# Kernel optimization log

Measured on AMD Instinct MI355X. Metric: run time of the kernel, lower is better.

Reference implementation:

```python
import jax, jax.numpy as jnp
import numpy as np

D = 4096


def ste_sign(v):
    # forward: sign(v); backward: identity (straight-through)
    return v + jax.lax.stop_gradient(jnp.sign(v) - v)


def setup_inputs() -> dict:
    key = jax.random.key(0)
    ks = jax.random.split(key, 7)
    B, T = 2, 4096
    x = jax.random.normal(ks[0], (B, T, D), dtype=jnp.float32)
    role_write = jax.random.normal(ks[1], (D,), dtype=jnp.float32) * 0.02
    role_read = jax.random.normal(ks[2], (D,), dtype=jnp.float32) * 0.02
    # nn.Linear(D, 1): weight (1, D) stored here as (D,), bias scalar (1,)
    lim = 1.0 / np.sqrt(D)
    wg_w = jax.random.uniform(ks[3], (D,), dtype=jnp.float32, minval=-lim, maxval=lim)
    wg_b = jax.random.uniform(ks[4], (1,), dtype=jnp.float32, minval=-lim, maxval=lim)
    rg_w = jax.random.uniform(ks[5], (D,), dtype=jnp.float32, minval=-lim, maxval=lim)
    rg_b = jax.random.uniform(ks[6], (1,), dtype=jnp.float32, minval=-lim, maxval=lim)
    return {"x": x, "role_write": role_write, "role_read": role_read,
            "wg_w": wg_w, "wg_b": wg_b, "rg_w": rg_w, "rg_b": rg_b}


def reference(x, role_write, role_read, wg_w, wg_b, rg_w, rg_b):
    # ---- write: gated sign-bind facts, causal bundle via cumsum over T ----
    signs = ste_sign(x)                                  # (B,T,D)
    facts = signs * ste_sign(role_write)                 # bind with write role
    w_gate = jax.nn.sigmoid(jnp.einsum('btd,d->bt', x, wg_w) + wg_b[0])
    gated_facts = facts * w_gate[..., None]
    memory = jnp.cumsum(gated_facts, axis=1)             # (B,T,D) causal bundle
    # ---- read: unbind memory with query, gated residual add ----
    query = signs * ste_sign(role_read)
    retrieved = ste_sign(memory) * query
    r_gate = jax.nn.sigmoid(jnp.einsum('btd,d->bt', x, rg_w) + rg_b[0])
    return x + r_gate[..., None] * retrieved
```

## Files before the change

### kernel.cpp

```cpp
#include <hip/hip_runtime.h>
#include <math.h>


#define T_LEN 4096
#define D_LEN 4096
#define TC 32
#define NC (T_LEN / TC)
#define D4 (D_LEN / 4)

typedef float nfloat4 __attribute__((ext_vector_type(4)));

__device__ __forceinline__ float fsgn(float v) {
    return (v > 0.f) ? 1.f : ((v < 0.f) ? -1.f : 0.f);
}
__device__ __forceinline__ double dsgn(double v) {
    return (v > 0.) ? 1. : ((v < 0.) ? -1. : 0.);
}
__device__ __forceinline__ unsigned scode(float v) {
    return (v > 0.f) ? 2u : ((v < 0.f) ? 0u : 1u);
}

__global__ __launch_bounds__(1024) void gates_partial_kernel(
    const float* __restrict__ x,
    const float* __restrict__ wg_w, const float* __restrict__ wg_b,
    const float* __restrict__ rg_w, const float* __restrict__ rg_b,
    double* __restrict__ wgate, double* __restrict__ rgate,
    double* __restrict__ partial)
{
    const int c = blockIdx.x;
    const int b = blockIdx.y;
    const int tid = threadIdx.x;

    __shared__ unsigned char codes[TC][D4];
    __shared__ double wg_s[TC];
    __shared__ double rg_s[TC];

    const int r  = tid >> 5;
    const int k0 = tid & 31;
    const float4* xr = (const float4*)(x + ((size_t)b * T_LEN + (size_t)c * TC + r) * D_LEN);
    const float4* w4 = (const float4*)wg_w;
    const float4* g4 = (const float4*)rg_w;

    double dw = 0., dg = 0.;
    #pragma unroll 4
    for (int j = 0; j < 32; ++j) {
        const int idx = k0 + j * 32;
        float4 v = xr[idx];
        float4 a = w4[idx];
        float4 g = g4[idx];
        dw += (double)v.x * a.x + (double)v.y * a.y
            + (double)v.z * a.z + (double)v.w * a.w;
        dg += (double)v.x * g.x + (double)v.y * g.y
            + (double)v.z * g.z + (double)v.w * g.w;
        codes[r][idx] = (unsigned char)(scode(v.x) | (scode(v.y) << 2)
                                      | (scode(v.z) << 4) | (scode(v.w) << 6));
    }
    #pragma unroll
    for (int off = 16; off >= 1; off >>= 1) {
        dw += __shfl_down(dw, off, 32);
        dg += __shfl_down(dg, off, 32);
    }
    if (k0 == 0) {
        wg_s[r] = 1. / (1. + exp(-(dw + (double)wg_b[0])));
        rg_s[r] = 1. / (1. + exp(-(dg + (double)rg_b[0])));
    }
    __syncthreads();

    if (tid < TC) {
        const int row = b * T_LEN + c * TC + tid;
        wgate[row] = wg_s[tid];
        rgate[row] = rg_s[tid];
    }

    double a0 = 0., a1 = 0., a2 = 0., a3 = 0.;
    #pragma unroll 8
    for (int t = 0; t < TC; ++t) {
        unsigned code = codes[t][tid];
        double w = wg_s[t];
        a0 += (double)((int)( code       & 3u) - 1) * w;
        a1 += (double)((int)((code >> 2) & 3u) - 1) * w;
        a2 += (double)((int)((code >> 4) & 3u) - 1) * w;
        a3 += (double)((int)((code >> 6) & 3u) - 1) * w;
    }
    double* rec = partial + ((size_t)(b * NC + c)) * D_LEN + tid * 4;
    rec[0] = a0; rec[1] = a1; rec[2] = a2; rec[3] = a3;
}

__global__ __launch_bounds__(256) void prefix_kernel(
    const double* __restrict__ partial, double* __restrict__ prefix)
{
    const int m = blockIdx.x * 256 + threadIdx.x;
    const int b = blockIdx.y;
    double s = 0.;
    for (int c = 0; c < NC; ++c) {
        size_t idx = ((size_t)(b * NC + c)) * D_LEN + m;
        double v = partial[idx];
        prefix[idx] = s;
        s += v;
    }
}

__global__ __launch_bounds__(256) void final_kernel(
    const float* __restrict__ x,
    const double* __restrict__ wgate, const double* __restrict__ rgate,
    const float* __restrict__ role_w, const float* __restrict__ role_r,
    const double* __restrict__ prefix,
    float* __restrict__ out)
{
    const int b = blockIdx.z;
    const int c = blockIdx.y;
    const int d4 = blockIdx.x * 256 + threadIdx.x;

    __shared__ double wsm[TC];
    __shared__ float rsm[TC];
    if (threadIdx.x < TC) {
        wsm[threadIdx.x] = wgate[b * T_LEN + c * TC + threadIdx.x];
        rsm[threadIdx.x] = (float)rgate[b * T_LEN + c * TC + threadIdx.x];
    }
    __syncthreads();

    float4 rw = ((const float4*)role_w)[d4];
    float4 rr = ((const float4*)role_r)[d4];
    const float kx = fsgn(rw.x) * fsgn(rr.x);
    const float ky = fsgn(rw.y) * fsgn(rr.y);
    const float kz = fsgn(rw.z) * fsgn(rr.z);
    const float kw = fsgn(rw.w) * fsgn(rr.w);

    const double* p = prefix + ((size_t)(b * NC + c)) * D_LEN + d4 * 4;
    double ax = p[0], ay = p[1], az = p[2], aw = p[3];

    const float4* x4 = (const float4*)x;
    nfloat4* o4 = (nfloat4*)out;
    const size_t slab = ((size_t)b * T_LEN + (size_t)c * TC) * D4 + d4;

    #pragma unroll 4
    for (int i = 0; i < TC; ++i) {
        float4 v = x4[slab + (size_t)i * D4];
        double w = wsm[i];
        float rf = rsm[i];
        float sx = fsgn(v.x), sy = fsgn(v.y), sz = fsgn(v.z), sw2 = fsgn(v.w);
        ax += (double)sx * w; ay += (double)sy * w;
        az += (double)sz * w; aw += (double)sw2 * w;
        nfloat4 o;
        o.x = v.x + rf * kx * (float)dsgn(ax) * sx;
        o.y = v.y + rf * ky * (float)dsgn(ay) * sy;
        o.z = v.z + rf * kz * (float)dsgn(az) * sz;
        o.w = v.w + rf * kw * (float)dsgn(aw) * sw2;
        __builtin_nontemporal_store(o, &o4[slab + (size_t)i * D4]);
    }
}

extern "C" void kernel_launch(void* const* d_in, const int* in_sizes, int n_in,
                              void* d_out, int out_size, void* d_ws, size_t ws_size,
                              hipStream_t stream) {
    const float* x      = (const float*)d_in[0];
    const float* role_w = (const float*)d_in[1];
    const float* role_r = (const float*)d_in[2];
    const float* wg_w   = (const float*)d_in[3];
    const float* wg_b   = (const float*)d_in[4];
    const float* rg_w   = (const float*)d_in[5];
    const float* rg_b   = (const float*)d_in[6];
    float* out = (float*)d_out;

    const int B = in_sizes[0] / (T_LEN * D_LEN);
    const int BT = B * T_LEN;

    double* wgate   = (double*)d_ws;
    double* rgate   = wgate + BT;
    double* partial = rgate + BT;
    double* prefix  = partial + (size_t)B * NC * D_LEN;

    dim3 g12(NC, B);
    gates_partial_kernel<<<g12, 1024, 0, stream>>>(
        x, wg_w, wg_b, rg_w, rg_b, wgate, rgate, partial);

    dim3 g2b(D_LEN / 256, B);
    prefix_kernel<<<g2b, 256, 0, stream>>>(partial, prefix);

    dim3 g3(D4 / 256, NC, B);
    final_kernel<<<g3, 256, 0, stream>>>(
        x, wgate, rgate, role_w, role_r, prefix, out);
}
```

Before: 88.82 us.

## Halve time-chunk size and parallelize chunk prefix scan across sections

Chunk length drops from 32 to 16 rows, so the gates/partial kernel launches twice as many blocks, each handling 16 rows with a full 64-lane wavefront per row. The prefix kernel, which walked all chunks serially with one thread per column, now splits the chunks into 8 sections per column. Each section is summed independently, combined with a shuffle scan, and then written. The aim is to expose more parallelism in the serial prefix pass, at the cost of twice the partial/prefix workspace traffic and two reads of partial in the scan.

```diff
diff --git a/kernel.cpp b/kernel.cpp
--- a/kernel.cpp
+++ b/kernel.cpp
@@ -4,9 +4,11 @@
 
 #define T_LEN 4096
 #define D_LEN 4096
-#define TC 32
+#define TC 16
 #define NC (T_LEN / TC)
 #define D4 (D_LEN / 4)
+#define NSEC 8
+#define SEC (NC / NSEC)
 
 typedef float nfloat4 __attribute__((ext_vector_type(4)));
 
@@ -35,16 +37,16 @@
     __shared__ double wg_s[TC];
     __shared__ double rg_s[TC];
 
-    const int r  = tid >> 5;
-    const int k0 = tid & 31;
+    const int r    = tid >> 6;
+    const int lane = tid & 63;
     const float4* xr = (const float4*)(x + ((size_t)b * T_LEN + (size_t)c * TC + r) * D_LEN);
     const float4* w4 = (const float4*)wg_w;
     const float4* g4 = (const float4*)rg_w;
 
     double dw = 0., dg = 0.;
     #pragma unroll 4
-    for (int j = 0; j < 32; ++j) {
-        const int idx = k0 + j * 32;
+    for (int j = 0; j < D4 / 64; ++j) {
+        const int idx = lane + j * 64;
         float4 v = xr[idx];
         float4 a = w4[idx];
         float4 g = g4[idx];
@@ -56,11 +58,11 @@
                                       | (scode(v.z) << 4) | (scode(v.w) << 6));
     }
     #pragma unroll
-    for (int off = 16; off >= 1; off >>= 1) {
-        dw += __shfl_down(dw, off, 32);
-        dg += __shfl_down(dg, off, 32);
-    }
-    if (k0 == 0) {
+    for (int off = 32; off >= 1; off >>= 1) {
+        dw += __shfl_down(dw, off);
+        dg += __shfl_down(dg, off);
+    }
+    if (lane == 0) {
         wg_s[r] = 1. / (1. + exp(-(dw + (double)wg_b[0])));
         rg_s[r] = 1. / (1. + exp(-(dg + (double)rg_b[0])));
     }
@@ -86,17 +88,37 @@
     rec[0] = a0; rec[1] = a1; rec[2] = a2; rec[3] = a3;
 }
 
-__global__ __launch_bounds__(256) void prefix_kernel(
+__global__ __launch_bounds__(1024) void prefix_kernel(
     const double* __restrict__ partial, double* __restrict__ prefix)
 {
-    const int m = blockIdx.x * 256 + threadIdx.x;
-    const int b = blockIdx.y;
+    const int tid  = threadIdx.x;
+    const int col8 = tid >> 3;
+    const int sec  = tid & 7;
+    const int g    = blockIdx.x * 128 + col8;
+    const int b    = g >> 12;
+    const int m    = g & 4095;
+
     double s = 0.;
-    for (int c = 0; c < NC; ++c) {
-        size_t idx = ((size_t)(b * NC + c)) * D_LEN + m;
+    #pragma unroll 8
+    for (int k = 0; k < SEC; ++k) {
+        const int cc = sec * SEC + k;
+        s += partial[((size_t)(b * NC + cc)) * D_LEN + m];
+    }
+    double inc = s;
+    #pragma unroll
+    for (int off = 1; off < NSEC; off <<= 1) {
+        double n = __shfl_up(inc, off, NSEC);
+        if (sec >= off) inc += n;
+    }
+    double run = __shfl_up(inc, 1, NSEC);
+    if (sec == 0) run = 0.;
+    #pragma unroll 8
+    for (int k = 0; k < SEC; ++k) {
+        const int cc = sec * SEC + k;
+        const size_t idx = ((size_t)(b * NC + cc)) * D_LEN + m;
         double v = partial[idx];
-        prefix[idx] = s;
-        s += v;
+        prefix[idx] = run;
+        run += v;
     }
 }
 
@@ -174,8 +196,8 @@
     gates_partial_kernel<<<g12, 1024, 0, stream>>>(
         x, wg_w, wg_b, rg_w, rg_b, wgate, rgate, partial);
 
-    dim3 g2b(D_LEN / 256, B);
-    prefix_kernel<<<g2b, 256, 0, stream>>>(partial, prefix);
+    const int ncols = B * D_LEN;
+    prefix_kernel<<<ncols / 128, 1024, 0, stream>>>(partial, prefix);
 
     dim3 g3(D4 / 256, NC, B);
     final_kernel<<<g3, 256, 0, stream>>>(
```

Result: slower. 122.3 us (+37.7%).
